# Kernel tuning notes

Hardware: AMD Instinct MI355X
Metric: run time of the kernel (lower is better)

Reference implementation:

```python
import jax, jax.numpy as jnp
import numpy as np

NA, NB, C = 50000, 50000, 128
E = 800000
S, IN, H, NBASES = 8, 64, 64, 8
NUM_LAYERS = 2
EPS = 1e-5


def setup_inputs() -> dict:
    key = jax.random.key(0)
    ks = jax.random.split(key, 16)
    inp = {
        'x_a': jax.random.normal(ks[0], (NA, C), jnp.float32),
        'x_b': jax.random.normal(ks[1], (NB, C), jnp.float32),
        'schema_x': jax.random.normal(ks[2], (S, IN), jnp.float32),
        'edge_ab': jax.random.randint(ks[3], (2, E), 0, NA, jnp.int32),
        'edge_ba': jax.random.randint(ks[4], (2, E), 0, NA, jnp.int32),
        'edge_aa': jax.random.randint(ks[5], (2, E), 0, NA, jnp.int32),
        'schema_edge_index': jax.random.randint(ks[6], (2, 24), 0, S, jnp.int32),
        'pre_W': jax.random.normal(ks[7], (H, IN), jnp.float32) * (1.0 / np.sqrt(IN)),
        'pre_b': jnp.zeros((H,), jnp.float32),
        'gcn_W': jax.random.normal(ks[8], (H, H), jnp.float32) * (1.0 / np.sqrt(H)),
        'gcn_b': jnp.zeros((H,), jnp.float32),
        'coeff_W': jax.random.normal(ks[9], (NBASES, 2 * H), jnp.float32) * (1.0 / np.sqrt(2 * H)),
        'coeff_b': jnp.zeros((NBASES,), jnp.float32),
        'bases': jax.random.normal(ks[10], (NUM_LAYERS, NBASES, C, C), jnp.float32) * (1.0 / np.sqrt(C)),
        'sage_bias': jnp.zeros((NUM_LAYERS, 3, C), jnp.float32),
        'ln_w': jnp.ones((NUM_LAYERS, 2, C), jnp.float32),
        'ln_b': jnp.zeros((NUM_LAYERS, 2, C), jnp.float32),
    }
    return inp


def _gcn_conv(x, ei, W, b):
    # PyG GCNConv: add self-loops, symmetric normalization, then linear.
    n = x.shape[0]
    loop = jnp.arange(n, dtype=ei.dtype)
    src = jnp.concatenate([ei[0], loop])
    dst = jnp.concatenate([ei[1], loop])
    deg = jax.ops.segment_sum(jnp.ones_like(dst, jnp.float32), dst, num_segments=n)
    dinv = jax.lax.rsqrt(jnp.maximum(deg, 1e-12))
    norm = dinv[src] * dinv[dst]  # [E+n]
    xw = x @ W.T  # [n, H]
    out = jax.ops.segment_sum(xw[src] * norm[:, None], dst, num_segments=n)
    return out + b


def _sage_conv(x_src, x_dst, ei, W, b):
    # PyG SAGEConv, aggr='mean': lin_l(mean_j x_src[j]) + lin_r(x_dst); lin_l.weight == lin_r.weight == W.
    n_dst = x_dst.shape[0]
    msg_sum = jax.ops.segment_sum(x_src[ei[0]], ei[1], num_segments=n_dst)
    cnt = jax.ops.segment_sum(jnp.ones(ei.shape[1], x_src.dtype), ei[1], num_segments=n_dst)
    mean = msg_sum / jnp.maximum(cnt, 1.0)[:, None]
    return (mean + x_dst) @ W.T + b


def _layer_norm(x, w, b):
    mu = jnp.mean(x, axis=-1, keepdims=True)
    var = jnp.mean(jnp.square(x - mu), axis=-1, keepdims=True)
    return (x - mu) * jax.lax.rsqrt(var + EPS) * w + b


def _edge_weight(sf_src, sf_dst, coeff_W, coeff_b, bases_l):
    combined = jnp.concatenate([sf_src, sf_dst], axis=0)  # [2H]
    coeffs = combined @ coeff_W.T + coeff_b  # [NBASES]
    return jnp.einsum('i,ijk->jk', coeffs, bases_l)  # [C, C]


def reference(x_a, x_b, schema_x, edge_ab, edge_ba, edge_aa, schema_edge_index,
              pre_W, pre_b, gcn_W, gcn_b, coeff_W, coeff_b, bases,
              sage_bias, ln_w, ln_b):
    # Schema GCN over the tiny table-level graph. table_to_index: a->0, b->1.
    h = schema_x @ pre_W.T + pre_b
    ori = h
    sf = jax.nn.relu(_gcn_conv(h, schema_edge_index, gcn_W, gcn_b))  # [S, H]

    for l in range(NUM_LAYERS):
        bases_l = bases[l]
        W_ab = _edge_weight(sf[0], sf[1], coeff_W, coeff_b, bases_l)
        W_ba = _edge_weight(sf[1], sf[0], coeff_W, coeff_b, bases_l)
        W_aa = _edge_weight(sf[0], sf[0], coeff_W, coeff_b, bases_l)
        # HeteroConv(aggr='sum'): sum SAGE outputs per destination node type.
        out_b = _sage_conv(x_a, x_b, edge_ab, W_ab, sage_bias[l, 0])
        out_a = (_sage_conv(x_b, x_a, edge_ba, W_ba, sage_bias[l, 1])
                 + _sage_conv(x_a, x_a, edge_aa, W_aa, sage_bias[l, 2]))
        x_a = jax.nn.relu(_layer_norm(out_a, ln_w[l, 0], ln_b[l, 0]))
        x_b = jax.nn.relu(_layer_norm(out_b, ln_w[l, 1], ln_b[l, 1]))

    return x_a, x_b, sf, ori
```

## Files before the change

### kernel.cpp

```cpp
#include <hip/hip_runtime.h>

#define NA 50000
#define NB 50000
#define NN 50000
#define CDIM 128
#define EDGES 800000
#define SS 8
#define INDIM 64
#define HDIM 64
#define NBASES 8
#define NBUCK 98
#define BSH 9

#define RROWS 32
#define USTR 136
#define SSTR 129

typedef __attribute__((ext_vector_type(8))) short bf16x8;
typedef __attribute__((ext_vector_type(4))) float f32x4;


__device__ __forceinline__ unsigned short f2bf(float f) {
    unsigned u = __float_as_uint(f);
    return (unsigned short)((u + 0x7FFFu + ((u >> 16) & 1u)) >> 16);
}

__global__ __launch_bounds__(512) void schema_kernel(
    const float* __restrict__ schema_x, const int* __restrict__ sei,
    const float* __restrict__ preW, const float* __restrict__ preb,
    const float* __restrict__ gcnW, const float* __restrict__ gcnb,
    const float* __restrict__ coW, const float* __restrict__ cob,
    float* __restrict__ out_sf, float* __restrict__ out_ori,
    float* __restrict__ coeffs)
{
    __shared__ float h[SS][HDIM];
    __shared__ float xw[SS][HDIM];
    __shared__ float sf[SS][HDIM];
    __shared__ float deg[SS];
    __shared__ float nrm[32];
    __shared__ int es[32], ed[32];

    int t = threadIdx.x;
    int i = t >> 6, j = t & 63;

    float acc = preb[j];
    for (int k = 0; k < INDIM; k++) acc += schema_x[i * INDIM + k] * preW[j * INDIM + k];
    h[i][j] = acc;
    out_ori[i * HDIM + j] = acc;
    if (t < SS) deg[t] = 0.0f;
    __syncthreads();

    if (t < 32) {
        int s, d;
        if (t < 24) { s = sei[t]; d = sei[24 + t]; }
        else        { s = t - 24; d = t - 24; }
        es[t] = s; ed[t] = d;
        atomicAdd(&deg[d], 1.0f);
    }
    __syncthreads();
    if (t < 32) {
        nrm[t] = rsqrtf(fmaxf(deg[es[t]], 1e-12f)) * rsqrtf(fmaxf(deg[ed[t]], 1e-12f));
    }
    float a2 = 0.0f;
    for (int k = 0; k < HDIM; k++) a2 += h[i][k] * gcnW[j * HDIM + k];
    xw[i][j] = a2;
    __syncthreads();

    float o = gcnb[j];
    for (int e = 0; e < 32; e++) {
        if (ed[e] == i) o += xw[es[e]][j] * nrm[e];
    }
    float s = fmaxf(o, 0.0f);
    sf[i][j] = s;
    out_sf[i * HDIM + j] = s;
    __syncthreads();

    if (t < 24) {
        int ty = t >> 3, ii = t & 7;
        int srow = (ty == 1) ? 1 : 0;
        int drow = (ty == 0) ? 1 : 0;
        float a = cob[ii];
        for (int k = 0; k < HDIM; k++) a += sf[srow][k] * coW[ii * (2 * HDIM) + k];
        for (int k = 0; k < HDIM; k++) a += sf[drow][k] * coW[ii * (2 * HDIM) + HDIM + k];
        coeffs[ty * 8 + ii] = a;
    }
}

__global__ __launch_bounds__(256) void build_w_kernel(
    const float* __restrict__ bases, const float* __restrict__ coeffs,
    unsigned short* __restrict__ Wbf)
{
    int idx = blockIdx.x * blockDim.x + threadIdx.x;
    int lt = idx >> 14;
    int jk = idx & 16383;
    int l = lt / 3, ty = lt % 3;
    float acc = 0.0f;
#pragma unroll
    for (int i = 0; i < NBASES; i++)
        acc += coeffs[ty * 8 + i] * bases[((size_t)(l * NBASES + i) << 14) + jk];
    Wbf[idx] = f2bf(acc);
}

__global__ __launch_bounds__(256) void tobf16_kernel(
    const float* __restrict__ in, unsigned short* __restrict__ out, int n)
{
    int i = (blockIdx.x * 256 + threadIdx.x) * 4;
    if (i >= n) return;
    float4 f = *(const float4*)(in + i);
    ushort4 o;
    o.x = f2bf(f.x); o.y = f2bf(f.y); o.z = f2bf(f.z); o.w = f2bf(f.w);
    *(ushort4*)(out + i) = o;
}

__global__ __launch_bounds__(256) void zero_rows_kernel(
    unsigned short* a0, unsigned short* b0, unsigned short* a1, unsigned short* b1)
{
    int t = threadIdx.x;
    int tab = t >> 6, w = t & 63;
    unsigned short* p = (tab == 0) ? a0 : (tab == 1) ? b0 : (tab == 2) ? a1 : b1;
    ((unsigned*)(p + (size_t)NN * CDIM))[w] = 0u;
}


__global__ __launch_bounds__(256) void bucket_count_kernel(
    const int* __restrict__ ab, const int* __restrict__ ba,
    const int* __restrict__ aa, int* __restrict__ bcnt)
{
    __shared__ int h[NBUCK];
    int t = threadIdx.x;
    int ty = blockIdx.y;
    const int* ei = (ty == 0) ? ab : (ty == 1) ? ba : aa;
    if (t < NBUCK) h[t] = 0;
    __syncthreads();
    int cb = blockIdx.x * 4096;
    int en = min(cb + 4096, EDGES);
    for (int e = cb + t; e < en; e += 256)
        atomicAdd(&h[ei[EDGES + e] >> BSH], 1);
    __syncthreads();
    if (t < NBUCK) atomicAdd(&bcnt[ty * NBUCK + t], h[t]);
}

__global__ __launch_bounds__(32) void bucket_scan_kernel(
    const int* __restrict__ bcnt, int* __restrict__ boff, int* __restrict__ bcur)
{
    int t = threadIdx.x;
    if (t < 3) {
        int run = 0;
        for (int i = 0; i < NBUCK; i++) {
            int c = bcnt[t * NBUCK + i];
            boff[t * (NBUCK + 1) + i] = run;
            bcur[t * NBUCK + i] = run;
            run += c;
        }
        boff[t * (NBUCK + 1) + NBUCK] = run;
    }
}

__global__ __launch_bounds__(256) void bucket_partition_kernel(
    const int* __restrict__ ab, const int* __restrict__ ba,
    const int* __restrict__ aa, int* __restrict__ bcur,
    unsigned* __restrict__ buf)
{
    __shared__ int h[NBUCK];
    __shared__ int basearr[NBUCK];
    __shared__ int cur[NBUCK];
    int t = threadIdx.x;
    int ty = blockIdx.y;
    const int* ei = (ty == 0) ? ab : (ty == 1) ? ba : aa;
    if (t < NBUCK) h[t] = 0;
    __syncthreads();
    int cb = blockIdx.x * 4096;
    int en = min(cb + 4096, EDGES);
    for (int e = cb + t; e < en; e += 256)
        atomicAdd(&h[ei[EDGES + e] >> BSH], 1);
    __syncthreads();
    if (t < NBUCK) {
        basearr[t] = atomicAdd(&bcur[ty * NBUCK + t], h[t]);
        cur[t] = 0;
    }
    __syncthreads();
    for (int e = cb + t; e < en; e += 256) {
        int src = ei[e], dst = ei[EDGES + e];
        int b = dst >> BSH;
        int r = atomicAdd(&cur[b], 1);
        buf[(size_t)ty * EDGES + basearr[b] + r] =
            ((unsigned)(dst & 511) << 16) | (unsigned)src;
    }
}

__global__ __launch_bounds__(256) void bucket_scatter_kernel(
    const unsigned* __restrict__ buf, const int* __restrict__ boff,
    int* __restrict__ rowptr, int* __restrict__ col)
{
    __shared__ int cnt[512];
    __shared__ int part[256];
    int t = threadIdx.x;
    int b = blockIdx.x, ty = blockIdx.y;
    int nstart = boff[ty * (NBUCK + 1) + b];
    int nend   = boff[ty * (NBUCK + 1) + b + 1];
    int n = nend - nstart;
    cnt[t] = 0; cnt[t + 256] = 0;
    __syncthreads();
    const unsigned* bb = buf + (size_t)ty * EDGES + nstart;
    for (int i = t; i < n; i += 256)
        atomicAdd(&cnt[bb[i] >> 16], 1);
    __syncthreads();
    int a0 = cnt[2 * t], a1 = cnt[2 * t + 1];
    int s = a0 + a1;
    part[t] = s;
    __syncthreads();
    for (int off = 1; off < 256; off <<= 1) {
        int v = (t >= off) ? part[t - off] : 0;
        __syncthreads();
        part[t] += v;
        __syncthreads();
    }
    int excl = part[t] - s;
    int p0 = excl, p1 = excl + a0;
    cnt[2 * t] = p0; cnt[2 * t + 1] = p1;
    int row0 = (b << BSH) + 2 * t;
    int rbase = ty * (NN + 1);
    if (row0 < NN)     rowptr[rbase + row0] = nstart + p0;
    if (row0 + 1 < NN) rowptr[rbase + row0 + 1] = nstart + p1;
    if (b == NBUCK - 1 && t == 255) rowptr[rbase + NN] = EDGES;
    __syncthreads();
    int* cc = col + (size_t)ty * EDGES + nstart;
    for (int i = t; i < n; i += 256) {
        unsigned pk = bb[i];
        int r = atomicAdd(&cnt[pk >> 16], 1);
        cc[r] = (int)(pk & 0xFFFFu);
    }
}


#define ACC4(gv, vv)                                            \
    gv.x += __uint_as_float((vv).x << 16);                      \
    gv.y += __uint_as_float((vv).x & 0xffff0000u);              \
    gv.z += __uint_as_float((vv).y << 16);                      \
    gv.w += __uint_as_float((vv).y & 0xffff0000u);

__global__ __launch_bounds__(256, 4) void fuse_b_kernel(
    const unsigned short* __restrict__ xsrc, const float* __restrict__ xdst,
    const int* __restrict__ rowptr, const int* __restrict__ col,
    const unsigned short* __restrict__ Wbf, const float* __restrict__ bias,
    const float* __restrict__ lnw, const float* __restrict__ lnb,
    float* __restrict__ xnext, unsigned short* __restrict__ xnext_bf)
{
    __shared__ float4 smraw[1032];
    unsigned short* Ubf = (unsigned short*)smraw;
    float* stage = (float*)smraw;
    int t = threadIdx.x;
    int base = blockIdx.x * RROWS;
    int wv = t >> 6;
    int lane = t & 63;
    int half = lane >> 5, cl = lane & 31;
    int off = cl << 2;

    for (int k = 0; k < 4; k++) {
        int rA = (2 * k) * 4 + wv;
        int rB = rA + 4;
        int rowA = base + rA, rowB = base + rB;
        int sA = 0, eA = 0, sB = 0, eB = 0;
        if (rowA < NN) { sA = rowptr[rowA]; eA = rowptr[rowA + 1]; }
        if (rowB < NN) { sB = rowptr[rowB]; eB = rowptr[rowB + 1]; }
        int csA[16], csB[16];
#pragma unroll
        for (int j = 0; j < 16; j++) {
            int sl = sA + 2 * j + half;
            int cc = col[min(sl, EDGES - 1)];
            csA[j] = (sl < eA) ? cc : NN;
        }
#pragma unroll
        for (int j = 0; j < 16; j++) {
            int sl = sB + 2 * j + half;
            int cc = col[min(sl, EDGES - 1)];
            csB[j] = (sl < eB) ? cc : NN;
        }
        uint2 vA[16], vB[16];
#pragma unroll
        for (int j = 0; j < 16; j++)
            vA[j] = *(const uint2*)(xsrc + (size_t)csA[j] * CDIM + off);
#pragma unroll
        for (int j = 0; j < 16; j++)
            vB[j] = *(const uint2*)(xsrc + (size_t)csB[j] * CDIM + off);
        float4 gA = make_float4(0.f, 0.f, 0.f, 0.f);
        float4 gB = make_float4(0.f, 0.f, 0.f, 0.f);
#pragma unroll
        for (int j = 0; j < 16; j++) { ACC4(gA, vA[j]) }
#pragma unroll
        for (int j = 0; j < 16; j++) { ACC4(gB, vB[j]) }
        for (int b2 = sA + 32; b2 < eA; b2 += 16) {
#pragma unroll
            for (int j = 0; j < 8; j++) {
                int sl = b2 + 2 * j + half;
                int cc = col[min(sl, EDGES - 1)];
                int id = (sl < eA) ? cc : NN;
                uint2 vv = *(const uint2*)(xsrc + (size_t)id * CDIM + off);
                ACC4(gA, vv)
            }
        }
        for (int b2 = sB + 32; b2 < eB; b2 += 16) {
#pragma unroll
            for (int j = 0; j < 8; j++) {
                int sl = b2 + 2 * j + half;
                int cc = col[min(sl, EDGES - 1)];
                int id = (sl < eB) ? cc : NN;
                uint2 vv = *(const uint2*)(xsrc + (size_t)id * CDIM + off);
                ACC4(gB, vv)
            }
        }
        gA.x += __shfl_xor(gA.x, 32, 64);
        gA.y += __shfl_xor(gA.y, 32, 64);
        gA.z += __shfl_xor(gA.z, 32, 64);
        gA.w += __shfl_xor(gA.w, 32, 64);
        gB.x += __shfl_xor(gB.x, 32, 64);
        gB.y += __shfl_xor(gB.y, 32, 64);
        gB.z += __shfl_xor(gB.z, 32, 64);
        gB.w += __shfl_xor(gB.w, 32, 64);
        if (half == 0) {
            ushort4 oA = make_ushort4(0, 0, 0, 0), oB = oA;
            if (rowA < NN) {
                float inv = 1.0f / (float)max(eA - sA, 1);
                const float4 xv = *(const float4*)(xdst + (size_t)rowA * CDIM + off);
                oA.x = f2bf(gA.x * inv + xv.x);
                oA.y = f2bf(gA.y * inv + xv.y);
                oA.z = f2bf(gA.z * inv + xv.z);
                oA.w = f2bf(gA.w * inv + xv.w);
            }
            if (rowB < NN) {
                float inv = 1.0f / (float)max(eB - sB, 1);
                const float4 xv = *(const float4*)(xdst + (size_t)rowB * CDIM + off);
                oB.x = f2bf(gB.x * inv + xv.x);
                oB.y = f2bf(gB.y * inv + xv.y);
                oB.z = f2bf(gB.z * inv + xv.z);
                oB.w = f2bf(gB.w * inv + xv.w);
            }
            *(ushort4*)&Ubf[rA * USTR + off] = oA;
            *(ushort4*)&Ubf[rB * USTR + off] = oB;
        }
    }
    __syncthreads();

    int qd = lane >> 4;
    int ln16 = lane & 15;
    f32x4 acc00 = {0.f,0.f,0.f,0.f}, acc01 = acc00, acc10 = acc00, acc11 = acc00;
#pragma unroll
    for (int ks = 0; ks < 4; ks++) {
        int koff = ks * 32 + qd * 8;
        bf16x8 a0 = *(const bf16x8*)&Ubf[(ln16) * USTR + koff];
        bf16x8 a1 = *(const bf16x8*)&Ubf[(16 + ln16) * USTR + koff];
        bf16x8 b0 = *(const bf16x8*)&Wbf[(size_t)((2 * wv + 0) * 16 + ln16) * CDIM + koff];
        bf16x8 b1 = *(const bf16x8*)&Wbf[(size_t)((2 * wv + 1) * 16 + ln16) * CDIM + koff];
        acc00 = __builtin_amdgcn_mfma_f32_16x16x32_bf16(a0, b0, acc00, 0, 0, 0);
        acc01 = __builtin_amdgcn_mfma_f32_16x16x32_bf16(a0, b1, acc01, 0, 0, 0);
        acc10 = __builtin_amdgcn_mfma_f32_16x16x32_bf16(a1, b0, acc10, 0, 0, 0);
        acc11 = __builtin_amdgcn_mfma_f32_16x16x32_bf16(a1, b1, acc11, 0, 0, 0);
    }
    __syncthreads();
    {
        int c0 = (2 * wv + 0) * 16 + ln16;
        int c1 = (2 * wv + 1) * 16 + ln16;
#pragma unroll
        for (int i = 0; i < 4; i++) {
            int r0 = qd * 4 + i;
            stage[r0 * SSTR + c0] = acc00[i];
            stage[r0 * SSTR + c1] = acc01[i];
            stage[(16 + r0) * SSTR + c0] = acc10[i];
            stage[(16 + r0) * SSTR + c1] = acc11[i];
        }
    }
    __syncthreads();

    float b0v = bias[lane], b1v = bias[lane + 64];
    float lw0 = lnw[lane], lw1 = lnw[lane + 64];
    float lb0 = lnb[lane], lb1 = lnb[lane + 64];
    for (int rr = 0; rr < RROWS / 4; rr++) {
        int r = rr * 4 + wv;
        int row = base + r;
        if (row >= NN) continue;
        float v0 = stage[r * SSTR + lane] + b0v;
        float v1 = stage[r * SSTR + lane + 64] + b1v;
        float s = v0 + v1, s2 = v0 * v0 + v1 * v1;
#pragma unroll
        for (int o2 = 32; o2 > 0; o2 >>= 1) {
            s  += __shfl_xor(s,  o2, 64);
            s2 += __shfl_xor(s2, o2, 64);
        }
        float mu = s * (1.0f / CDIM);
        float var = s2 * (1.0f / CDIM) - mu * mu;
        float rs = rsqrtf(var + 1e-5f);
        float o0 = fmaxf((v0 - mu) * rs * lw0 + lb0, 0.0f);
        float o1 = fmaxf((v1 - mu) * rs * lw1 + lb1, 0.0f);
        size_t oi = (size_t)row * CDIM;
        xnext[oi + lane] = o0;
        xnext[oi + lane + 64] = o1;
        if (xnext_bf) {
            xnext_bf[oi + lane] = f2bf(o0);
            xnext_bf[oi + lane + 64] = f2bf(o1);
        }
    }
}

__global__ __launch_bounds__(256, 4) void fuse_a_kernel(
    const unsigned short* __restrict__ xsrc1, const int* __restrict__ rowptr1, const int* __restrict__ col1,
    const unsigned short* __restrict__ xsrc2, const int* __restrict__ rowptr2, const int* __restrict__ col2,
    const float* __restrict__ xdst,
    const unsigned short* __restrict__ W1bf, const unsigned short* __restrict__ W2bf,
    const float* __restrict__ bias1, const float* __restrict__ bias2,
    const float* __restrict__ lnw, const float* __restrict__ lnb,
    float* __restrict__ xnext, unsigned short* __restrict__ xnext_bf)
{
    __shared__ float4 smraw[1088];
    unsigned short* Ubf = (unsigned short*)smraw;
    unsigned short* Vbf = Ubf + RROWS * USTR;
    float* stage = (float*)smraw;
    int t = threadIdx.x;
    int base = blockIdx.x * RROWS;
    int wv = t >> 6;
    int lane = t & 63;
    int half = lane >> 5, cl = lane & 31;
    int off = cl << 2;

    for (int rr = 0; rr < 8; rr++) {
        int r = rr * 4 + wv;
        int row = base + r;
        int s1 = 0, e1 = 0, s2 = 0, e2 = 0;
        if (row < NN) {
            s1 = rowptr1[row]; e1 = rowptr1[row + 1];
            s2 = rowptr2[row]; e2 = rowptr2[row + 1];
        }
        int cs1[16], cs2[16];
#pragma unroll
        for (int j = 0; j < 16; j++) {
            int sl = s1 + 2 * j + half;
            int cc = col1[min(sl, EDGES - 1)];
            cs1[j] = (sl < e1) ? cc : NN;
        }
#pragma unroll
        for (int j = 0; j < 16; j++) {
            int sl = s2 + 2 * j + half;
            int cc = col2[min(sl, EDGES - 1)];
            cs2[j] = (sl < e2) ? cc : NN;
        }
        uint2 v1[16], v2[16];
#pragma unroll
        for (int j = 0; j < 16; j++)
            v1[j] = *(const uint2*)(xsrc1 + (size_t)cs1[j] * CDIM + off);
#pragma unroll
        for (int j = 0; j < 16; j++)
            v2[j] = *(const uint2*)(xsrc2 + (size_t)cs2[j] * CDIM + off);
        float4 g1 = make_float4(0.f, 0.f, 0.f, 0.f);
        float4 g2 = make_float4(0.f, 0.f, 0.f, 0.f);
#pragma unroll
        for (int j = 0; j < 16; j++) { ACC4(g1, v1[j]) }
#pragma unroll
        for (int j = 0; j < 16; j++) { ACC4(g2, v2[j]) }
        for (int b2 = s1 + 32; b2 < e1; b2 += 16) {
#pragma unroll
            for (int j = 0; j < 8; j++) {
                int sl = b2 + 2 * j + half;
                int cc = col1[min(sl, EDGES - 1)];
                int id = (sl < e1) ? cc : NN;
                uint2 vv = *(const uint2*)(xsrc1 + (size_t)id * CDIM + off);
                ACC4(g1, vv)
            }
        }
        for (int b2 = s2 + 32; b2 < e2; b2 += 16) {
#pragma unroll
            for (int j = 0; j < 8; j++) {
                int sl = b2 + 2 * j + half;
                int cc = col2[min(sl, EDGES - 1)];
                int id = (sl < e2) ? cc : NN;
                uint2 vv = *(const uint2*)(xsrc2 + (size_t)id * CDIM + off);
                ACC4(g2, vv)
            }
        }
        g1.x += __shfl_xor(g1.x, 32, 64);
        g1.y += __shfl_xor(g1.y, 32, 64);
        g1.z += __shfl_xor(g1.z, 32, 64);
        g1.w += __shfl_xor(g1.w, 32, 64);
        g2.x += __shfl_xor(g2.x, 32, 64);
        g2.y += __shfl_xor(g2.y, 32, 64);
        g2.z += __shfl_xor(g2.z, 32, 64);
        g2.w += __shfl_xor(g2.w, 32, 64);
        if (half == 0) {
            ushort4 ou = make_ushort4(0, 0, 0, 0), ov = ou;
            if (row < NN) {
                const float4 xv = *(const float4*)(xdst + (size_t)row * CDIM + off);
                float i1 = 1.0f / (float)max(e1 - s1, 1);
                float i2 = 1.0f / (float)max(e2 - s2, 1);
                ou.x = f2bf(g1.x * i1 + xv.x); ou.y = f2bf(g1.y * i1 + xv.y);
                ou.z = f2bf(g1.z * i1 + xv.z); ou.w = f2bf(g1.w * i1 + xv.w);
                ov.x = f2bf(g2.x * i2 + xv.x); ov.y = f2bf(g2.y * i2 + xv.y);
                ov.z = f2bf(g2.z * i2 + xv.z); ov.w = f2bf(g2.w * i2 + xv.w);
            }
            *(ushort4*)&Ubf[r * USTR + off] = ou;
            *(ushort4*)&Vbf[r * USTR + off] = ov;
        }
    }
    __syncthreads();

    int qd = lane >> 4;
    int ln16 = lane & 15;
    f32x4 acc00 = {0.f,0.f,0.f,0.f}, acc01 = acc00, acc10 = acc00, acc11 = acc00;
#pragma unroll
    for (int ks = 0; ks < 4; ks++) {
        int koff = ks * 32 + qd * 8;
        bf16x8 aU0 = *(const bf16x8*)&Ubf[(ln16) * USTR + koff];
        bf16x8 aU1 = *(const bf16x8*)&Ubf[(16 + ln16) * USTR + koff];
        bf16x8 aV0 = *(const bf16x8*)&Vbf[(ln16) * USTR + koff];
        bf16x8 aV1 = *(const bf16x8*)&Vbf[(16 + ln16) * USTR + koff];
        size_t wrow0 = (size_t)((2 * wv + 0) * 16 + ln16) * CDIM + koff;
        size_t wrow1 = (size_t)((2 * wv + 1) * 16 + ln16) * CDIM + koff;
        bf16x8 b10 = *(const bf16x8*)&W1bf[wrow0];
        bf16x8 b11 = *(const bf16x8*)&W1bf[wrow1];
        bf16x8 b20 = *(const bf16x8*)&W2bf[wrow0];
        bf16x8 b21 = *(const bf16x8*)&W2bf[wrow1];
        acc00 = __builtin_amdgcn_mfma_f32_16x16x32_bf16(aU0, b10, acc00, 0, 0, 0);
        acc01 = __builtin_amdgcn_mfma_f32_16x16x32_bf16(aU0, b11, acc01, 0, 0, 0);
        acc10 = __builtin_amdgcn_mfma_f32_16x16x32_bf16(aU1, b10, acc10, 0, 0, 0);
        acc11 = __builtin_amdgcn_mfma_f32_16x16x32_bf16(aU1, b11, acc11, 0, 0, 0);
        acc00 = __builtin_amdgcn_mfma_f32_16x16x32_bf16(aV0, b20, acc00, 0, 0, 0);
        acc01 = __builtin_amdgcn_mfma_f32_16x16x32_bf16(aV0, b21, acc01, 0, 0, 0);
        acc10 = __builtin_amdgcn_mfma_f32_16x16x32_bf16(aV1, b20, acc10, 0, 0, 0);
        acc11 = __builtin_amdgcn_mfma_f32_16x16x32_bf16(aV1, b21, acc11, 0, 0, 0);
    }
    __syncthreads();
    {
        int c0 = (2 * wv + 0) * 16 + ln16;
        int c1 = (2 * wv + 1) * 16 + ln16;
#pragma unroll
        for (int i = 0; i < 4; i++) {
            int r0 = qd * 4 + i;
            stage[r0 * SSTR + c0] = acc00[i];
            stage[r0 * SSTR + c1] = acc01[i];
            stage[(16 + r0) * SSTR + c0] = acc10[i];
            stage[(16 + r0) * SSTR + c1] = acc11[i];
        }
    }
    __syncthreads();

    float b0v = bias1[lane] + bias2[lane];
    float b1v = bias1[lane + 64] + bias2[lane + 64];
    float lw0 = lnw[lane], lw1 = lnw[lane + 64];
    float lb0 = lnb[lane], lb1 = lnb[lane + 64];
    for (int rr = 0; rr < RROWS / 4; rr++) {
        int r = rr * 4 + wv;
        int row = base + r;
        if (row >= NN) continue;
        float v0 = stage[r * SSTR + lane] + b0v;
        float v1 = stage[r * SSTR + lane + 64] + b1v;
        float s = v0 + v1, s2 = v0 * v0 + v1 * v1;
#pragma unroll
        for (int o2 = 32; o2 > 0; o2 >>= 1) {
            s  += __shfl_xor(s,  o2, 64);
            s2 += __shfl_xor(s2, o2, 64);
        }
        float mu = s * (1.0f / CDIM);
        float var = s2 * (1.0f / CDIM) - mu * mu;
        float rs = rsqrtf(var + 1e-5f);
        float o0 = fmaxf((v0 - mu) * rs * lw0 + lb0, 0.0f);
        float o1 = fmaxf((v1 - mu) * rs * lw1 + lb1, 0.0f);
        size_t oi = (size_t)row * CDIM;
        xnext[oi + lane] = o0;
        xnext[oi + lane + 64] = o1;
        if (xnext_bf) {
            xnext_bf[oi + lane] = f2bf(o0);
            xnext_bf[oi + lane + 64] = f2bf(o1);
        }
    }
}

extern "C" void kernel_launch(void* const* d_in, const int* in_sizes, int n_in,
                              void* d_out, int out_size, void* d_ws, size_t ws_size,
                              hipStream_t stream)
{
    const float* x_a      = (const float*)d_in[0];
    const float* x_b      = (const float*)d_in[1];
    const float* schema_x = (const float*)d_in[2];
    const int*   e_ab     = (const int*)d_in[3];
    const int*   e_ba     = (const int*)d_in[4];
    const int*   e_aa     = (const int*)d_in[5];
    const int*   sei      = (const int*)d_in[6];
    const float* preW     = (const float*)d_in[7];
    const float* preb     = (const float*)d_in[8];
    const float* gcnW     = (const float*)d_in[9];
    const float* gcnb     = (const float*)d_in[10];
    const float* coW      = (const float*)d_in[11];
    const float* cob      = (const float*)d_in[12];
    const float* bases    = (const float*)d_in[13];
    const float* sbias    = (const float*)d_in[14];
    const float* lnw      = (const float*)d_in[15];
    const float* lnb      = (const float*)d_in[16];

    float* out     = (float*)d_out;
    float* out_xa  = out;
    float* out_xb  = out + 6400000;
    float* out_sf  = out + 12800000;
    float* out_ori = out + 12800512;

    float* ws = (float*)d_ws;
    int*      col    = (int*)ws;
    int*      rowptr = (int*)(ws + 2400000);
    unsigned* buf    = (unsigned*)(ws + 2550016);
    int*      bcnt   = (int*)(ws + 4950016);
    int*      boff   = (int*)(ws + 4950320);
    int*      bcur   = (int*)(ws + 4950624);
    float* xa_buf = ws + 4950928;
    float* xb_buf = ws + 11350928;
    unsigned short* Wbf = (unsigned short*)(ws + 17750928);
    float* coeffs = ws + 17800080;
    unsigned short* xa_bf0 = (unsigned short*)(ws + 17800112);
    unsigned short* xb_bf0 = (unsigned short*)(ws + 21000176);
    unsigned short* xa_bf1 = (unsigned short*)(ws + 24200240);
    unsigned short* xb_bf1 = (unsigned short*)(ws + 27400304);

    schema_kernel<<<1, 512, 0, stream>>>(schema_x, sei, preW, preb, gcnW, gcnb,
                                         coW, cob, out_sf, out_ori, coeffs);
    build_w_kernel<<<384, 256, 0, stream>>>(bases, coeffs, Wbf);

    tobf16_kernel<<<(NA * CDIM / 4 + 255) / 256, 256, 0, stream>>>(x_a, xa_bf0, NA * CDIM);
    tobf16_kernel<<<(NB * CDIM / 4 + 255) / 256, 256, 0, stream>>>(x_b, xb_bf0, NB * CDIM);
    zero_rows_kernel<<<1, 256, 0, stream>>>(xa_bf0, xb_bf0, xa_bf1, xb_bf1);

    hipMemsetAsync(bcnt, 0, 3 * NBUCK * sizeof(int), stream);
    dim3 cgrid((EDGES + 4095) / 4096, 3);
    bucket_count_kernel<<<cgrid, 256, 0, stream>>>(e_ab, e_ba, e_aa, bcnt);
    bucket_scan_kernel<<<1, 32, 0, stream>>>(bcnt, boff, bcur);
    bucket_partition_kernel<<<cgrid, 256, 0, stream>>>(e_ab, e_ba, e_aa, bcur, buf);
    dim3 sgrid(NBUCK, 3);
    bucket_scatter_kernel<<<sgrid, 256, 0, stream>>>(buf, boff, rowptr, col);

    const int* rp_ab = rowptr;
    const int* rp_ba = rowptr + (NN + 1);
    const int* rp_aa = rowptr + 2 * (NN + 1);
    const int* col_ab = col;
    const int* col_ba = col + EDGES;
    const int* col_aa = col + 2 * EDGES;

    const int fgrid = (NN + RROWS - 1) / RROWS;

    for (int l = 0; l < 2; l++) {
        const float* xa_cur = (l == 0) ? x_a : xa_buf;
        const float* xb_cur = (l == 0) ? x_b : xb_buf;
        const unsigned short* xa_bf = (l == 0) ? xa_bf0 : xa_bf1;
        const unsigned short* xb_bf = (l == 0) ? xb_bf0 : xb_bf1;
        const unsigned short* Wab = Wbf + (size_t)(l * 3 + 0) * 16384;
        const unsigned short* Wba = Wbf + (size_t)(l * 3 + 1) * 16384;
        const unsigned short* Waa = Wbf + (size_t)(l * 3 + 2) * 16384;
        float* xa_nxt = (l == 0) ? xa_buf : out_xa;
        float* xb_nxt = (l == 0) ? xb_buf : out_xb;
        unsigned short* xa_nbf = (l == 0) ? xa_bf1 : nullptr;
        unsigned short* xb_nbf = (l == 0) ? xb_bf1 : nullptr;

        fuse_b_kernel<<<fgrid, 256, 0, stream>>>(
            xa_bf, xb_cur, rp_ab, col_ab, Wab,
            sbias + (size_t)(l * 3 + 0) * 128,
            lnw + (size_t)(l * 2 + 1) * 128, lnb + (size_t)(l * 2 + 1) * 128,
            xb_nxt, xb_nbf);
        fuse_a_kernel<<<fgrid, 256, 0, stream>>>(
            xb_bf, rp_ba, col_ba, xa_bf, rp_aa, col_aa, xa_cur,
            Wba, Waa,
            sbias + (size_t)(l * 3 + 1) * 128, sbias + (size_t)(l * 3 + 2) * 128,
            lnw + (size_t)(l * 2 + 0) * 128, lnb + (size_t)(l * 2 + 0) * 128,
            xa_nxt, xa_nbf);
    }
}
```

Measured before the change: 576.5 us.

## Merge per-layer A/B SAGE kernels into one launch and read bf16 root features

Combines fuse_a and fuse_b into a single kernel whose even blocks handle type-a rows and odd blocks handle type-b rows, so both node types are processed in one launch per layer. The root (x_dst) term is now read from the bf16 copies instead of fp32, and the layer-0 fp32 intermediate outputs are no longer written. The two bf16 conversion launches are also merged into one 2D grid. This cuts launch count and memory traffic, but adds extra rounding on the root term and mixes blocks with uneven work in one grid.

```diff
diff --git a/kernel.cpp b/kernel.cpp
--- a/kernel.cpp
+++ b/kernel.cpp
@@ -102,8 +102,11 @@
 }
 
 __global__ __launch_bounds__(256) void tobf16_kernel(
-    const float* __restrict__ in, unsigned short* __restrict__ out, int n)
-{
+    const float* __restrict__ ina, const float* __restrict__ inb,
+    unsigned short* __restrict__ outa, unsigned short* __restrict__ outb, int n)
+{
+    const float* in = blockIdx.y ? inb : ina;
+    unsigned short* out = blockIdx.y ? outb : outa;
     int i = (blockIdx.x * 256 + threadIdx.x) * 4;
     if (i >= n) return;
     float4 f = *(const float4*)(in + i);
@@ -239,18 +242,16 @@
     gv.z += __uint_as_float((vv).y << 16);                      \
     gv.w += __uint_as_float((vv).y & 0xffff0000u);
 
-__global__ __launch_bounds__(256, 4) void fuse_b_kernel(
-    const unsigned short* __restrict__ xsrc, const float* __restrict__ xdst,
+__device__ __forceinline__ void fuse_b_body(
+    float4* smraw, int base, int t,
+    const unsigned short* __restrict__ xsrc, const unsigned short* __restrict__ xdst,
     const int* __restrict__ rowptr, const int* __restrict__ col,
     const unsigned short* __restrict__ Wbf, const float* __restrict__ bias,
     const float* __restrict__ lnw, const float* __restrict__ lnb,
     float* __restrict__ xnext, unsigned short* __restrict__ xnext_bf)
 {
-    __shared__ float4 smraw[1032];
     unsigned short* Ubf = (unsigned short*)smraw;
     float* stage = (float*)smraw;
-    int t = threadIdx.x;
-    int base = blockIdx.x * RROWS;
     int wv = t >> 6;
     int lane = t & 63;
     int half = lane >> 5, cl = lane & 31;
@@ -321,19 +322,19 @@
             ushort4 oA = make_ushort4(0, 0, 0, 0), oB = oA;
             if (rowA < NN) {
                 float inv = 1.0f / (float)max(eA - sA, 1);
-                const float4 xv = *(const float4*)(xdst + (size_t)rowA * CDIM + off);
-                oA.x = f2bf(gA.x * inv + xv.x);
-                oA.y = f2bf(gA.y * inv + xv.y);
-                oA.z = f2bf(gA.z * inv + xv.z);
-                oA.w = f2bf(gA.w * inv + xv.w);
+                uint2 xv = *(const uint2*)(xdst + (size_t)rowA * CDIM + off);
+                oA.x = f2bf(gA.x * inv + __uint_as_float(xv.x << 16));
+                oA.y = f2bf(gA.y * inv + __uint_as_float(xv.x & 0xffff0000u));
+                oA.z = f2bf(gA.z * inv + __uint_as_float(xv.y << 16));
+                oA.w = f2bf(gA.w * inv + __uint_as_float(xv.y & 0xffff0000u));
             }
             if (rowB < NN) {
                 float inv = 1.0f / (float)max(eB - sB, 1);
-                const float4 xv = *(const float4*)(xdst + (size_t)rowB * CDIM + off);
-                oB.x = f2bf(gB.x * inv + xv.x);
-                oB.y = f2bf(gB.y * inv + xv.y);
-                oB.z = f2bf(gB.z * inv + xv.z);
-                oB.w = f2bf(gB.w * inv + xv.w);
+                uint2 xv = *(const uint2*)(xdst + (size_t)rowB * CDIM + off);
+                oB.x = f2bf(gB.x * inv + __uint_as_float(xv.x << 16));
+                oB.y = f2bf(gB.y * inv + __uint_as_float(xv.x & 0xffff0000u));
+                oB.z = f2bf(gB.z * inv + __uint_as_float(xv.y << 16));
+                oB.w = f2bf(gB.w * inv + __uint_as_float(xv.y & 0xffff0000u));
             }
             *(ushort4*)&Ubf[rA * USTR + off] = oA;
             *(ushort4*)&Ubf[rB * USTR + off] = oB;
@@ -392,8 +393,10 @@
         float o0 = fmaxf((v0 - mu) * rs * lw0 + lb0, 0.0f);
         float o1 = fmaxf((v1 - mu) * rs * lw1 + lb1, 0.0f);
         size_t oi = (size_t)row * CDIM;
-        xnext[oi + lane] = o0;
-        xnext[oi + lane + 64] = o1;
+        if (xnext) {
+            xnext[oi + lane] = o0;
+            xnext[oi + lane + 64] = o1;
+        }
         if (xnext_bf) {
             xnext_bf[oi + lane] = f2bf(o0);
             xnext_bf[oi + lane + 64] = f2bf(o1);
@@ -401,21 +404,19 @@
     }
 }
 
-__global__ __launch_bounds__(256, 4) void fuse_a_kernel(
+__device__ __forceinline__ void fuse_a_body(
+    float4* smraw, int base, int t,
     const unsigned short* __restrict__ xsrc1, const int* __restrict__ rowptr1, const int* __restrict__ col1,
     const unsigned short* __restrict__ xsrc2, const int* __restrict__ rowptr2, const int* __restrict__ col2,
-    const float* __restrict__ xdst,
+    const unsigned short* __restrict__ xdst,
     const unsigned short* __restrict__ W1bf, const unsigned short* __restrict__ W2bf,
     const float* __restrict__ bias1, const float* __restrict__ bias2,
     const float* __restrict__ lnw, const float* __restrict__ lnb,
     float* __restrict__ xnext, unsigned short* __restrict__ xnext_bf)
 {
-    __shared__ float4 smraw[1088];
     unsigned short* Ubf = (unsigned short*)smraw;
     unsigned short* Vbf = Ubf + RROWS * USTR;
     float* stage = (float*)smraw;
-    int t = threadIdx.x;
-    int base = blockIdx.x * RROWS;
     int wv = t >> 6;
     int lane = t & 63;
     int half = lane >> 5, cl = lane & 31;
@@ -486,13 +487,17 @@
         if (half == 0) {
             ushort4 ou = make_ushort4(0, 0, 0, 0), ov = ou;
             if (row < NN) {
-                const float4 xv = *(const float4*)(xdst + (size_t)row * CDIM + off);
+                uint2 xv = *(const uint2*)(xdst + (size_t)row * CDIM + off);
+                float x0 = __uint_as_float(xv.x << 16);
+                float x1 = __uint_as_float(xv.x & 0xffff0000u);
+                float x2 = __uint_as_float(xv.y << 16);
+                float x3 = __uint_as_float(xv.y & 0xffff0000u);
                 float i1 = 1.0f / (float)max(e1 - s1, 1);
                 float i2 = 1.0f / (float)max(e2 - s2, 1);
-                ou.x = f2bf(g1.x * i1 + xv.x); ou.y = f2bf(g1.y * i1 + xv.y);
-                ou.z = f2bf(g1.z * i1 + xv.z); ou.w = f2bf(g1.w * i1 + xv.w);
-                ov.x = f2bf(g2.x * i2 + xv.x); ov.y = f2bf(g2.y * i2 + xv.y);
-                ov.z = f2bf(g2.z * i2 + xv.z); ov.w = f2bf(g2.w * i2 + xv.w);
+                ou.x = f2bf(g1.x * i1 + x0); ou.y = f2bf(g1.y * i1 + x1);
+                ou.z = f2bf(g1.z * i1 + x2); ou.w = f2bf(g1.w * i1 + x3);
+                ov.x = f2bf(g2.x * i2 + x0); ov.y = f2bf(g2.y * i2 + x1);
+                ov.z = f2bf(g2.z * i2 + x2); ov.w = f2bf(g2.w * i2 + x3);
             }
             *(ushort4*)&Ubf[r * USTR + off] = ou;
             *(ushort4*)&Vbf[r * USTR + off] = ov;
@@ -562,12 +567,41 @@
         float o0 = fmaxf((v0 - mu) * rs * lw0 + lb0, 0.0f);
         float o1 = fmaxf((v1 - mu) * rs * lw1 + lb1, 0.0f);
         size_t oi = (size_t)row * CDIM;
-        xnext[oi + lane] = o0;
-        xnext[oi + lane + 64] = o1;
+        if (xnext) {
+            xnext[oi + lane] = o0;
+            xnext[oi + lane + 64] = o1;
+        }
         if (xnext_bf) {
             xnext_bf[oi + lane] = f2bf(o0);
             xnext_bf[oi + lane + 64] = f2bf(o1);
         }
+    }
+}
+
+__global__ __launch_bounds__(256, 4) void fuse_ab_kernel(
+    const unsigned short* __restrict__ xa_bf, const unsigned short* __restrict__ xb_bf,
+    const int* __restrict__ rp_ab, const int* __restrict__ col_ab,
+    const int* __restrict__ rp_ba, const int* __restrict__ col_ba,
+    const int* __restrict__ rp_aa, const int* __restrict__ col_aa,
+    const unsigned short* __restrict__ Wab, const unsigned short* __restrict__ Wba,
+    const unsigned short* __restrict__ Waa,
+    const float* __restrict__ bias_ab, const float* __restrict__ bias_ba,
+    const float* __restrict__ bias_aa,
+    const float* __restrict__ lnw_a, const float* __restrict__ lnb_a,
+    const float* __restrict__ lnw_b, const float* __restrict__ lnb_b,
+    float* __restrict__ xa_out, unsigned short* __restrict__ xa_obf,
+    float* __restrict__ xb_out, unsigned short* __restrict__ xb_obf)
+{
+    __shared__ float4 smraw[1088];
+    int bid = blockIdx.x;
+    int base = (bid >> 1) * RROWS;
+    int t = threadIdx.x;
+    if (!(bid & 1)) {
+        fuse_a_body(smraw, base, t, xb_bf, rp_ba, col_ba, xa_bf, rp_aa, col_aa,
+                    xa_bf, Wba, Waa, bias_ba, bias_aa, lnw_a, lnb_a, xa_out, xa_obf);
+    } else {
+        fuse_b_body(smraw, base, t, xa_bf, xb_bf, rp_ab, col_ab,
+                    Wab, bias_ab, lnw_b, lnb_b, xb_out, xb_obf);
     }
 }
 
@@ -606,8 +640,6 @@
     int*      bcnt   = (int*)(ws + 4950016);
     int*      boff   = (int*)(ws + 4950320);
     int*      bcur   = (int*)(ws + 4950624);
-    float* xa_buf = ws + 4950928;
-    float* xb_buf = ws + 11350928;
     unsigned short* Wbf = (unsigned short*)(ws + 17750928);
     float* coeffs = ws + 17800080;
     unsigned short* xa_bf0 = (unsigned short*)(ws + 17800112);
@@ -619,8 +651,8 @@
                                          coW, cob, out_sf, out_ori, coeffs);
     build_w_kernel<<<384, 256, 0, stream>>>(bases, coeffs, Wbf);
 
-    tobf16_kernel<<<(NA * CDIM / 4 + 255) / 256, 256, 0, stream>>>(x_a, xa_bf0, NA * CDIM);
-    tobf16_kernel<<<(NB * CDIM / 4 + 255) / 256, 256, 0, stream>>>(x_b, xb_bf0, NB * CDIM);
+    dim3 tg((NA * CDIM / 4 + 255) / 256, 2);
+    tobf16_kernel<<<tg, 256, 0, stream>>>(x_a, x_b, xa_bf0, xb_bf0, NA * CDIM);
     zero_rows_kernel<<<1, 256, 0, stream>>>(xa_bf0, xb_bf0, xa_bf1, xb_bf1);
 
     hipMemsetAsync(bcnt, 0, 3 * NBUCK * sizeof(int), stream);
@@ -641,28 +673,24 @@
     const int fgrid = (NN + RROWS - 1) / RROWS;
 
     for (int l = 0; l < 2; l++) {
-        const float* xa_cur = (l == 0) ? x_a : xa_buf;
-        const float* xb_cur = (l == 0) ? x_b : xb_buf;
         const unsigned short* xa_bf = (l == 0) ? xa_bf0 : xa_bf1;
         const unsigned short* xb_bf = (l == 0) ? xb_bf0 : xb_bf1;
         const unsigned short* Wab = Wbf + (size_t)(l * 3 + 0) * 16384;
         const unsigned short* Wba = Wbf + (size_t)(l * 3 + 1) * 16384;
         const unsigned short* Waa = Wbf + (size_t)(l * 3 + 2) * 16384;
-        float* xa_nxt = (l == 0) ? xa_buf : out_xa;
-        float* xb_nxt = (l == 0) ? xb_buf : out_xb;
-        unsigned short* xa_nbf = (l == 0) ? xa_bf1 : nullptr;
-        unsigned short* xb_nbf = (l == 0) ? xb_bf1 : nullptr;
-
-        fuse_b_kernel<<<fgrid, 256, 0, stream>>>(
-            xa_bf, xb_cur, rp_ab, col_ab, Wab,
+        float* xa_out = (l == 0) ? nullptr : out_xa;
+        float* xb_out = (l == 0) ? nullptr : out_xb;
+        unsigned short* xa_obf = (l == 0) ? xa_bf1 : nullptr;
+        unsigned short* xb_obf = (l == 0) ? xb_bf1 : nullptr;
+
+        fuse_ab_kernel<<<2 * fgrid, 256, 0, stream>>>(
+            xa_bf, xb_bf, rp_ab, col_ab, rp_ba, col_ba, rp_aa, col_aa,
+            Wab, Wba, Waa,
             sbias + (size_t)(l * 3 + 0) * 128,
+            sbias + (size_t)(l * 3 + 1) * 128,
+            sbias + (size_t)(l * 3 + 2) * 128,
+            lnw + (size_t)(l * 2 + 0) * 128, lnb + (size_t)(l * 2 + 0) * 128,
             lnw + (size_t)(l * 2 + 1) * 128, lnb + (size_t)(l * 2 + 1) * 128,
-            xb_nxt, xb_nbf);
-        fuse_a_kernel<<<fgrid, 256, 0, stream>>>(
-            xb_bf, rp_ba, col_ba, xa_bf, rp_aa, col_aa, xa_cur,
-            Wba, Waa,
-            sbias + (size_t)(l * 3 + 1) * 128, sbias + (size_t)(l * 3 + 2) * 128,
-            lnw + (size_t)(l * 2 + 0) * 128, lnb + (size_t)(l * 2 + 0) * 128,
-            xa_nxt, xa_nbf);
-    }
-}
+            xa_out, xa_obf, xb_out, xb_obf);
+    }
+}
```

Result: slower. 598.2 us (+3.8%).
